# Optimization experiments

Measured on AMD Instinct MI355X. Metric: run time of the kernel, lower is better.

The kernel has to match this reference:

```python
import jax, jax.numpy as jnp
import numpy as np

B = 8192
T = 100       # repeat_vector
I = 30        # input_size
H = 100       # hidden_size


def setup_inputs() -> dict:
    key = jax.random.key(0)
    ks = jax.random.split(key, 7)
    k = 1.0 / np.sqrt(H)  # torch LSTM/Linear init scale
    u = lambda kk, shape: jax.random.uniform(kk, shape, jnp.float32, -k, k)
    return {
        "x": jax.random.normal(ks[0], (B, I), jnp.float32),
        "W_ih": u(ks[1], (4 * H, I)),   # gate order: i, f, g, o
        "W_hh": u(ks[2], (4 * H, H)),
        "b_ih": u(ks[3], (4 * H,)),
        "b_hh": u(ks[4], (4 * H,)),
        "W_d": u(ks[5], (1, H)),
        "b_d": u(ks[6], (1,)),
    }


def _lstm_dense(x, W_ih, W_hh, b_ih, b_hh, W_d, b_d):
    # Input is the same vector at every timestep (repeat), so project once.
    xp = x @ W_ih.T + b_ih + b_hh  # [B, 4H]
    h0 = jnp.zeros((x.shape[0], H), x.dtype)
    c0 = jnp.zeros((x.shape[0], H), x.dtype)

    def step(carry, _):
        h, c = carry
        gates = xp + h @ W_hh.T                      # [B, 4H]
        i, f, g, o = jnp.split(gates, 4, axis=-1)
        i = jax.nn.sigmoid(i)
        f = jax.nn.sigmoid(f)
        g = jnp.tanh(g)
        o = jax.nn.sigmoid(o)
        c = f * c + i * g
        h = o * jnp.tanh(c)
        return (h, c), h

    _, hs = jax.lax.scan(step, (h0, c0), None, length=T)  # [T, B, H]
    hs = jnp.transpose(hs, (1, 0, 2))                     # [B, T, H]
    return hs @ W_d.T + b_d                               # [B, T, 1]


def reference(x, W_ih, W_hh, b_ih, b_hh, W_d, b_d):
    return _lstm_dense(x, W_ih, W_hh, b_ih, b_hh, W_d, b_d)
```

## Files before the change

kernel.cpp:

```cpp
#include <hip/hip_runtime.h>


#define LOG2E 1.44269504088896340736f

typedef _Float16 f16x8 __attribute__((ext_vector_type(8)));
typedef float    f32x4 __attribute__((ext_vector_type(4)));

__device__ __forceinline__ float rcp_(float x) { return __builtin_amdgcn_rcpf(x); }
__device__ __forceinline__ float exp2_(float x) { return __builtin_amdgcn_exp2f(x); }

#define KS 136

__global__ __launch_bounds__(512, 4) void lstm_kernel(
    const float* __restrict__ x, const float* __restrict__ Wih,
    const float* __restrict__ Whh, const float* __restrict__ bih,
    const float* __restrict__ bhh, const float* __restrict__ Wd,
    const float* __restrict__ bd, float* __restrict__ out)
{
    __shared__ __align__(16) char smem[128 * KS * 2];
    __shared__ __align__(16) _Float16 hlds[2][16 * KS];
    __shared__ __align__(16) float xq_lds[8 * 4 * 64 * 4];

    _Float16* Wstg = (_Float16*)smem;
    float*    outb = (float*)smem;

    const int tid = threadIdx.x;
    const int w   = tid >> 6;
    const int l   = tid & 63;
    const int g   = l >> 4;
    const int c   = l & 15;
    const int b0  = blockIdx.x * 16;
    const int u   = w * 16 + c;

    for (int i = tid; i < 128 * KS / 2; i += 512) ((unsigned*)Wstg)[i] = 0u;
    for (int i = tid; i < 2 * 16 * KS / 2; i += 512) ((unsigned*)&hlds[0][0])[i] = 0u;
    __syncthreads();

    f16x8 wfrag[4][4];
    for (int s = 0; s < 4; ++s) {
        const float sc = (s == 2) ? (-2.0f * LOG2E) : (-LOG2E);
        for (int idx = tid; idx < 10000; idx += 512) {
            int uu = idx / 100, k = idx - uu * 100;
            Wstg[uu * KS + k] = (_Float16)(Whh[(s * 100 + uu) * 100 + k] * sc);
        }
        if (s == 0)
            for (int k = tid; k < 100; k += 512)
                Wstg[112 * KS + k] = (_Float16)Wd[k];
        __syncthreads();
        if (w < 7) {
            #pragma unroll
            for (int ks = 0; ks < 4; ++ks)
                wfrag[s][ks] = *(const f16x8*)&Wstg[u * KS + ks * 32 + g * 8];
        } else if (s == 0) {
            #pragma unroll
            for (int ks = 0; ks < 4; ++ks)
                wfrag[0][ks] = *(const f16x8*)&Wstg[(112 + c) * KS + ks * 32 + g * 8];
        }
        __syncthreads();
    }

    {
        float xq[4][4];
        #pragma unroll
        for (int s = 0; s < 4; ++s)
            #pragma unroll
            for (int r = 0; r < 4; ++r) xq[s][r] = 0.0f;
        if (w < 7 && u < 100) {
            for (int k = 0; k < 30; ++k) {
                float xv[4];
                #pragma unroll
                for (int r = 0; r < 4; ++r) xv[r] = x[(b0 + 4 * g + r) * 30 + k];
                #pragma unroll
                for (int s = 0; s < 4; ++s) {
                    float wv = Wih[(s * 100 + u) * 30 + k];
                    #pragma unroll
                    for (int r = 0; r < 4; ++r) xq[s][r] += xv[r] * wv;
                }
            }
            #pragma unroll
            for (int s = 0; s < 4; ++s) {
                float sc = (s == 2) ? (-2.0f * LOG2E) : (-LOG2E);
                float b  = bih[s * 100 + u] + bhh[s * 100 + u];
                #pragma unroll
                for (int r = 0; r < 4; ++r) xq[s][r] = (xq[s][r] + b) * sc;
            }
        }
        #pragma unroll
        for (int s = 0; s < 4; ++s) {
            f32x4 v = {xq[s][0], xq[s][1], xq[s][2], xq[s][3]};
            *(f32x4*)&xq_lds[(w * 4 + s) * 256 / 4 * 4 + l * 4 + 0] = v;
        }
    }
    const float bdv = bd[0];
    float creg[4] = {0.f, 0.f, 0.f, 0.f};
    __syncthreads();

    const int afb = c * KS + g * 8;
    const int xqb = w * 1024 + l * 4;
    const int hwb = u;

#define STEP(P, TCUR)                                                         \
    {                                                                         \
        const _Float16* hr = &hlds[(P)][0];                                   \
        _Float16*       hw = &hlds[(P) ^ 1][0];                               \
        f16x8 af[4];                                                          \
        _Pragma("unroll")                                                     \
        for (int ks = 0; ks < 4; ++ks)                                        \
            af[ks] = *(const f16x8*)&hr[afb + ks * 32];                       \
        if (w < 7) {                                                          \
            f32x4 acc[4];                                                     \
            _Pragma("unroll")                                                 \
            for (int s = 0; s < 4; ++s)                                       \
                acc[s] = *(const f32x4*)&xq_lds[xqb + s * 256];               \
            _Pragma("unroll")                                                 \
            for (int ks = 0; ks < 4; ++ks)                                    \
                _Pragma("unroll")                                             \
                for (int s = 0; s < 4; ++s)                                   \
                    acc[s] = __builtin_amdgcn_mfma_f32_16x16x32_f16(          \
                            af[ks], wfrag[s][ks], acc[s], 0, 0, 0);           \
            _Pragma("unroll")                                                 \
            for (int r = 0; r < 4; ++r) {                                     \
                float A  = exp2_(acc[0][r]);                                  \
                float F  = exp2_(acc[1][r]);                                  \
                float G  = exp2_(acc[2][r]);                                  \
                float O  = exp2_(acc[3][r]);                                  \
                float a1 = 1.0f + A, f1 = 1.0f + F;                           \
                float g1 = 1.0f + G, gm = 1.0f - G;                           \
                float ag  = a1 * g1;                                          \
                float num = fmaf(creg[r], ag, gm * f1);                       \
                float cg  = num * rcp_(ag * f1);                              \
                creg[r] = cg;                                                 \
                float C2 = exp2_(cg * (-2.0f * LOG2E));                       \
                float hv = (1.0f - C2) * rcp_((1.0f + O) * (1.0f + C2));      \
                hw[(4 * g + r) * KS + hwb] = (_Float16)hv;                    \
            }                                                                 \
        } else {                                                              \
            f32x4 a = {0.f, 0.f, 0.f, 0.f};                                   \
            _Pragma("unroll")                                                 \
            for (int ks = 0; ks < 4; ++ks)                                    \
                a = __builtin_amdgcn_mfma_f32_16x16x32_f16(                   \
                        af[ks], wfrag[0][ks], a, 0, 0, 0);                    \
            if ((TCUR) > 0 && c == 0) {                                       \
                _Pragma("unroll")                                             \
                for (int r = 0; r < 4; ++r)                                   \
                    outb[(4 * g + r) * 100 + (TCUR) - 1] = a[r] + bdv;        \
            }                                                                 \
        }                                                                     \
        __syncthreads();                                                      \
    }

    for (int t2 = 0; t2 < 50; ++t2) {
        STEP(0, 2 * t2);
        STEP(1, 2 * t2 + 1);
    }
#undef STEP

    if (w == 7) {
        f16x8 af[4];
        #pragma unroll
        for (int ks = 0; ks < 4; ++ks)
            af[ks] = *(const f16x8*)&hlds[0][afb + ks * 32];
        f32x4 a = {0.f, 0.f, 0.f, 0.f};
        #pragma unroll
        for (int ks = 0; ks < 4; ++ks)
            a = __builtin_amdgcn_mfma_f32_16x16x32_f16(af[ks], wfrag[0][ks], a, 0, 0, 0);
        if (c == 0) {
            #pragma unroll
            for (int r = 0; r < 4; ++r)
                outb[(4 * g + r) * 100 + 99] = a[r] + bdv;
        }
    }
    __syncthreads();

    {
        f32x4*       o4 = (f32x4*)(out + b0 * 100);
        const f32x4* s4 = (const f32x4*)outb;
        for (int i = tid; i < 400; i += 512) o4[i] = s4[i];
    }
}

extern "C" void kernel_launch(void* const* d_in, const int* in_sizes, int n_in,
                              void* d_out, int out_size, void* d_ws, size_t ws_size,
                              hipStream_t stream) {
    (void)in_sizes; (void)n_in; (void)out_size; (void)d_ws; (void)ws_size;
    const float* x   = (const float*)d_in[0];
    const float* Wih = (const float*)d_in[1];
    const float* Whh = (const float*)d_in[2];
    const float* bih = (const float*)d_in[3];
    const float* bhh = (const float*)d_in[4];
    const float* Wd  = (const float*)d_in[5];
    const float* bd  = (const float*)d_in[6];
    lstm_kernel<<<dim3(512), dim3(512), 0, stream>>>(
        x, Wih, Whh, bih, bhh, Wd, bd, (float*)d_out);
}
```

Before: 148.2 us.

## Fold input projection and dense head into augmented recurrent MFMA K dimension

Extends the recurrent K dimension with x and a constant-one column, so the input projection, biases and dense-head bias come out of the same MFMA. The separate xq LDS buffer and its per-step loads go away. The eighth wave dedicated to the dense output is also removed: the Wd row is placed in the unused hidden slot 101 and read by one lane of wave 6, so the block drops to 448 threads. Gate math is rewritten with paired float2 operations. The cost is a fifth MFMA per gate per step and fp16 precision for x, W_ih and the biases.

Result: slower. 154.3 us (+4.1%).

```diff
diff --git a/kernel.cpp b/kernel.cpp
--- a/kernel.cpp
+++ b/kernel.cpp
@@ -5,21 +5,21 @@
 
 typedef _Float16 f16x8 __attribute__((ext_vector_type(8)));
 typedef float    f32x4 __attribute__((ext_vector_type(4)));
+typedef float    f32x2 __attribute__((ext_vector_type(2)));
 
 __device__ __forceinline__ float rcp_(float x) { return __builtin_amdgcn_rcpf(x); }
 __device__ __forceinline__ float exp2_(float x) { return __builtin_amdgcn_exp2f(x); }
 
-#define KS 136
+#define KS2 168
 
-__global__ __launch_bounds__(512, 4) void lstm_kernel(
+__global__ __launch_bounds__(448, 4) void lstm_kernel(
     const float* __restrict__ x, const float* __restrict__ Wih,
     const float* __restrict__ Whh, const float* __restrict__ bih,
     const float* __restrict__ bhh, const float* __restrict__ Wd,
     const float* __restrict__ bd, float* __restrict__ out)
 {
-    __shared__ __align__(16) char smem[128 * KS * 2];
-    __shared__ __align__(16) _Float16 hlds[2][16 * KS];
-    __shared__ __align__(16) float xq_lds[8 * 4 * 64 * 4];
+    __shared__ __align__(16) char smem[128 * KS2 * 2];
+    __shared__ __align__(16) _Float16 hlds[2][16 * KS2];
 
     _Float16* Wstg = (_Float16*)smem;
     float*    outb = (float*)smem;
@@ -31,120 +31,98 @@
     const int c   = l & 15;
     const int b0  = blockIdx.x * 16;
     const int u   = w * 16 + c;
+    const bool wpo = (w == 6) && (c == 5);
 
-    for (int i = tid; i < 128 * KS / 2; i += 512) ((unsigned*)Wstg)[i] = 0u;
-    for (int i = tid; i < 2 * 16 * KS / 2; i += 512) ((unsigned*)&hlds[0][0])[i] = 0u;
+    for (int i = tid; i < 128 * KS2 / 2; i += 448) ((unsigned*)Wstg)[i] = 0u;
+    for (int i = tid; i < 2 * 16 * KS2 / 2; i += 448) ((unsigned*)&hlds[0][0])[i] = 0u;
     __syncthreads();
 
-    f16x8 wfrag[4][4];
+    for (int idx = tid; idx < 960; idx += 448) {
+        int buf = idx / 480, rem = idx - buf * 480;
+        int rr = rem / 30, kk = rem - rr * 30;
+        hlds[buf][rr * KS2 + 112 + kk] = (_Float16)x[(b0 + rr) * 30 + kk];
+    }
+    if (tid < 32) hlds[tid >> 4][(tid & 15) * KS2 + 142] = (_Float16)1.0f;
+
+    f16x8 wfrag[4][5];
     for (int s = 0; s < 4; ++s) {
         const float sc = (s == 2) ? (-2.0f * LOG2E) : (-LOG2E);
-        for (int idx = tid; idx < 10000; idx += 512) {
-            int uu = idx / 100, k = idx - uu * 100;
-            Wstg[uu * KS + k] = (_Float16)(Whh[(s * 100 + uu) * 100 + k] * sc);
+        for (int idx = tid; idx < 13100; idx += 448) {
+            if (idx < 10000) {
+                int uu = idx / 100, k = idx - uu * 100;
+                Wstg[uu * KS2 + k] = (_Float16)(Whh[(s * 100 + uu) * 100 + k] * sc);
+            } else if (idx < 13000) {
+                int j = idx - 10000, uu = j / 30, k = j - uu * 30;
+                Wstg[uu * KS2 + 112 + k] = (_Float16)(Wih[(s * 100 + uu) * 30 + k] * sc);
+            } else {
+                int uu = idx - 13000;
+                Wstg[uu * KS2 + 142] =
+                    (_Float16)((bih[s * 100 + uu] + bhh[s * 100 + uu]) * sc);
+            }
         }
-        if (s == 0)
-            for (int k = tid; k < 100; k += 512)
-                Wstg[112 * KS + k] = (_Float16)Wd[k];
+        if (s == 0) {
+            for (int k = tid; k < 100; k += 448)
+                Wstg[101 * KS2 + k] = (_Float16)Wd[k];
+            if (tid == 0) Wstg[101 * KS2 + 142] = (_Float16)bd[0];
+        }
         __syncthreads();
-        if (w < 7) {
-            #pragma unroll
-            for (int ks = 0; ks < 4; ++ks)
-                wfrag[s][ks] = *(const f16x8*)&Wstg[u * KS + ks * 32 + g * 8];
-        } else if (s == 0) {
-            #pragma unroll
-            for (int ks = 0; ks < 4; ++ks)
-                wfrag[0][ks] = *(const f16x8*)&Wstg[(112 + c) * KS + ks * 32 + g * 8];
-        }
+        #pragma unroll
+        for (int ks = 0; ks < 5; ++ks)
+            wfrag[s][ks] = *(const f16x8*)&Wstg[u * KS2 + ks * 32 + g * 8];
         __syncthreads();
     }
 
-    {
-        float xq[4][4];
-        #pragma unroll
-        for (int s = 0; s < 4; ++s)
-            #pragma unroll
-            for (int r = 0; r < 4; ++r) xq[s][r] = 0.0f;
-        if (w < 7 && u < 100) {
-            for (int k = 0; k < 30; ++k) {
-                float xv[4];
-                #pragma unroll
-                for (int r = 0; r < 4; ++r) xv[r] = x[(b0 + 4 * g + r) * 30 + k];
-                #pragma unroll
-                for (int s = 0; s < 4; ++s) {
-                    float wv = Wih[(s * 100 + u) * 30 + k];
-                    #pragma unroll
-                    for (int r = 0; r < 4; ++r) xq[s][r] += xv[r] * wv;
-                }
-            }
-            #pragma unroll
-            for (int s = 0; s < 4; ++s) {
-                float sc = (s == 2) ? (-2.0f * LOG2E) : (-LOG2E);
-                float b  = bih[s * 100 + u] + bhh[s * 100 + u];
-                #pragma unroll
-                for (int r = 0; r < 4; ++r) xq[s][r] = (xq[s][r] + b) * sc;
-            }
-        }
-        #pragma unroll
-        for (int s = 0; s < 4; ++s) {
-            f32x4 v = {xq[s][0], xq[s][1], xq[s][2], xq[s][3]};
-            *(f32x4*)&xq_lds[(w * 4 + s) * 256 / 4 * 4 + l * 4 + 0] = v;
-        }
-    }
-    const float bdv = bd[0];
-    float creg[4] = {0.f, 0.f, 0.f, 0.f};
+    f32x2 creg2[2] = {{0.f, 0.f}, {0.f, 0.f}};
     __syncthreads();
 
-    const int afb = c * KS + g * 8;
-    const int xqb = w * 1024 + l * 4;
-    const int hwb = u;
+    const int afb = c * KS2 + g * 8;
 
 #define STEP(P, TCUR)                                                         \
     {                                                                         \
         const _Float16* hr = &hlds[(P)][0];                                   \
         _Float16*       hw = &hlds[(P) ^ 1][0];                               \
-        f16x8 af[4];                                                          \
+        f32x4 acc[4];                                                         \
         _Pragma("unroll")                                                     \
-        for (int ks = 0; ks < 4; ++ks)                                        \
-            af[ks] = *(const f16x8*)&hr[afb + ks * 32];                       \
-        if (w < 7) {                                                          \
-            f32x4 acc[4];                                                     \
+        for (int s = 0; s < 4; ++s) acc[s] = (f32x4){0.f, 0.f, 0.f, 0.f};     \
+        _Pragma("unroll")                                                     \
+        for (int ks = 0; ks < 5; ++ks) {                                      \
+            f16x8 a = *(const f16x8*)&hr[afb + ks * 32];                      \
             _Pragma("unroll")                                                 \
             for (int s = 0; s < 4; ++s)                                       \
-                acc[s] = *(const f32x4*)&xq_lds[xqb + s * 256];               \
+                acc[s] = __builtin_amdgcn_mfma_f32_16x16x32_f16(              \
+                        a, wfrag[s][ks], acc[s], 0, 0, 0);                    \
+        }                                                                     \
+              \
+        if ((TCUR) > 0 && wpo) {                                              \
             _Pragma("unroll")                                                 \
-            for (int ks = 0; ks < 4; ++ks)                                    \
-                _Pragma("unroll")                                             \
-                for (int s = 0; s < 4; ++s)                                   \
-                    acc[s] = __builtin_amdgcn_mfma_f32_16x16x32_f16(          \
-                            af[ks], wfrag[s][ks], acc[s], 0, 0, 0);           \
-            _Pragma("unroll")                                                 \
-            for (int r = 0; r < 4; ++r) {                                     \
-                float A  = exp2_(acc[0][r]);                                  \
-                float F  = exp2_(acc[1][r]);                                  \
-                float G  = exp2_(acc[2][r]);                                  \
-                float O  = exp2_(acc[3][r]);                                  \
-                float a1 = 1.0f + A, f1 = 1.0f + F;                           \
-                float g1 = 1.0f + G, gm = 1.0f - G;                           \
-                float ag  = a1 * g1;                                          \
-                float num = fmaf(creg[r], ag, gm * f1);                       \
-                float cg  = num * rcp_(ag * f1);                              \
-                creg[r] = cg;                                                 \
-                float C2 = exp2_(cg * (-2.0f * LOG2E));                       \
-                float hv = (1.0f - C2) * rcp_((1.0f + O) * (1.0f + C2));      \
-                hw[(4 * g + r) * KS + hwb] = (_Float16)hv;                    \
-            }                                                                 \
-        } else {                                                              \
-            f32x4 a = {0.f, 0.f, 0.f, 0.f};                                   \
-            _Pragma("unroll")                                                 \
-            for (int ks = 0; ks < 4; ++ks)                                    \
-                a = __builtin_amdgcn_mfma_f32_16x16x32_f16(                   \
-                        af[ks], wfrag[0][ks], a, 0, 0, 0);                    \
-            if ((TCUR) > 0 && c == 0) {                                       \
-                _Pragma("unroll")                                             \
-                for (int r = 0; r < 4; ++r)                                   \
-                    outb[(4 * g + r) * 100 + (TCUR) - 1] = a[r] + bdv;        \
-            }                                                                 \
+            for (int r = 0; r < 4; ++r)                                       \
+                outb[(4 * g + r) * 100 + (TCUR) - 1] = acc[0][r];             \
+        }                                                                     \
+                                   \
+        _Pragma("unroll")                                                     \
+        for (int q = 0; q < 2; ++q) {                                         \
+            f32x2 A2 = {exp2_(acc[0][2 * q]), exp2_(acc[0][2 * q + 1])};      \
+            f32x2 F2 = {exp2_(acc[1][2 * q]), exp2_(acc[1][2 * q + 1])};      \
+            f32x2 G2 = {exp2_(acc[2][2 * q]), exp2_(acc[2][2 * q + 1])};      \
+            f32x2 O2 = {exp2_(acc[3][2 * q]), exp2_(acc[3][2 * q + 1])};      \
+            f32x2 a1 = A2 + 1.0f;                                             \
+            f32x2 f1 = F2 + 1.0f;                                             \
+            f32x2 g1 = G2 + 1.0f;                                             \
+            f32x2 gm = 1.0f - G2;                                             \
+            f32x2 ag = a1 * g1;                                               \
+            f32x2 num = creg2[q] * ag + gm * f1;                              \
+            f32x2 den = ag * f1;                                              \
+            f32x2 rd = {rcp_(den[0]), rcp_(den[1])};                          \
+            f32x2 cg = num * rd;                                              \
+            creg2[q] = cg;                                                    \
+            f32x2 cgk = cg * (-2.0f * LOG2E);                                 \
+            f32x2 C2 = {exp2_(cgk[0]), exp2_(cgk[1])};                        \
+            f32x2 c2m = 1.0f - C2;                                            \
+            f32x2 od = (O2 + 1.0f) * (C2 + 1.0f);                             \
+            f32x2 ro = {rcp_(od[0]), rcp_(od[1])};                            \
+            f32x2 hv = c2m * ro;                                              \
+            hw[(4 * g + 2 * q) * KS2 + u]     = (_Float16)hv[0];              \
+            hw[(4 * g + 2 * q + 1) * KS2 + u] = (_Float16)hv[1];              \
         }                                                                     \
         __syncthreads();                                                      \
     }
@@ -155,19 +133,17 @@
     }
 #undef STEP
 
-    if (w == 7) {
-        f16x8 af[4];
+    {
+        f32x4 a99 = {0.f, 0.f, 0.f, 0.f};
         #pragma unroll
-        for (int ks = 0; ks < 4; ++ks)
-            af[ks] = *(const f16x8*)&hlds[0][afb + ks * 32];
-        f32x4 a = {0.f, 0.f, 0.f, 0.f};
-        #pragma unroll
-        for (int ks = 0; ks < 4; ++ks)
-            a = __builtin_amdgcn_mfma_f32_16x16x32_f16(af[ks], wfrag[0][ks], a, 0, 0, 0);
-        if (c == 0) {
+        for (int ks = 0; ks < 5; ++ks) {
+            f16x8 a = *(const f16x8*)&hlds[0][afb + ks * 32];
+            a99 = __builtin_amdgcn_mfma_f32_16x16x32_f16(a, wfrag[0][ks], a99, 0, 0, 0);
+        }
+        if (wpo) {
             #pragma unroll
             for (int r = 0; r < 4; ++r)
-                outb[(4 * g + r) * 100 + 99] = a[r] + bdv;
+                outb[(4 * g + r) * 100 + 99] = a99[r];
         }
     }
     __syncthreads();
@@ -175,7 +151,7 @@
     {
         f32x4*       o4 = (f32x4*)(out + b0 * 100);
         const f32x4* s4 = (const f32x4*)outb;
-        for (int i = tid; i < 400; i += 512) o4[i] = s4[i];
+        for (int i = tid; i < 400; i += 448) o4[i] = s4[i];
     }
 }
 
@@ -190,6 +166,6 @@
     const float* bhh = (const float*)d_in[4];
     const float* Wd  = (const float*)d_in[5];
     const float* bd  = (const float*)d_in[6];
-    lstm_kernel<<<dim3(512), dim3(512), 0, stream>>>(
+    lstm_kernel<<<dim3(512), dim3(448), 0, stream>>>(
         x, Wih, Whh, bih, bhh, Wd, bd, (float*)d_out);
 }
```
